# Kernel tuning notes

Hardware: AMD Instinct MI355X
Metric: run time of the kernel (lower is better)

Reference implementation:

```python
import jax, jax.numpy as jnp
import numpy as np

EMBED = 128
VOCAB = 64


def setup_inputs() -> dict:
    key = jax.random.key(0)
    ks = jax.random.split(key, 7)
    B, L, V, E = 512, 1024, VOCAB, EMBED
    seq = jax.random.normal(ks[0], (B, L, V), dtype=jnp.float32)
    # Linear params (torch convention: weight [out, in])
    W_in = jax.random.normal(ks[1], (E, V), dtype=jnp.float32) / np.sqrt(V)
    b_in = jax.random.normal(ks[2], (E,), dtype=jnp.float32) * 0.01
    W_h = jax.random.normal(ks[3], (E, 2 * E), dtype=jnp.float32) / np.sqrt(2 * E)
    b_h = jax.random.normal(ks[4], (E,), dtype=jnp.float32) * 0.01
    W_out = jax.random.normal(ks[5], (V, E), dtype=jnp.float32) / np.sqrt(E)
    b_out = jax.random.normal(ks[6], (V,), dtype=jnp.float32) * 0.01
    return {"seq": seq, "W_in": W_in, "b_in": b_in, "W_h": W_h,
            "b_h": b_h, "W_out": W_out, "b_out": b_out}


def reference(seq, W_in, b_in, W_h, b_h, W_out, b_out):
    B, L, V = seq.shape
    E = W_in.shape[0]
    # Precompute input projection for all timesteps (equivalent to per-step _in)
    x_proj = jnp.einsum('blv,ev->ble', seq, W_in) + b_in  # [B, L, E]
    # concat([x, h]) @ W_h.T == x @ W_h[:, :E].T + h @ W_h[:, E:].T
    Wh_x = W_h[:, :E].T  # [E, E]
    Wh_h = W_h[:, E:].T  # [E, E]

    def step(h, x_t):
        h_new = jax.nn.relu(x_t @ Wh_x + h @ Wh_h + b_h)
        return h_new, None

    h0 = jnp.zeros((B, E), dtype=seq.dtype)
    xs = jnp.swapaxes(x_proj, 0, 1)  # [L, B, E]
    h_final, _ = jax.lax.scan(step, h0, xs)
    return h_final @ W_out.T + b_out  # [B, V]
```

## Files before the change

kernel.cpp:

```cpp
#include <hip/hip_runtime.h>
#include <hip/hip_bf16.h>

namespace {
constexpr int Bn = 512;
constexpr int Ln = 1024;
constexpr int Vn = 64;
constexpr int En = 128;
constexpr int Kc = Vn + En;
constexpr size_t SEQB_BYTES  = (size_t)Bn * Ln * Vn * 2;
constexpr size_t WALLB_BYTES = (size_t)En * Kc * 2;
constexpr size_t BC_BYTES    = En * 4;
constexpr size_t WOUTP_BYTES = (size_t)Vn * En * 2;
constexpr size_t FAST_WS  = SEQB_BYTES + WALLB_BYTES + BC_BYTES;
constexpr size_t FAST_WS2 = SEQB_BYTES + WALLB_BYTES + BC_BYTES + WOUTP_BYTES;
}

typedef __attribute__((ext_vector_type(8))) short bf16x8;
typedef __attribute__((ext_vector_type(4))) float f32x4;
typedef __attribute__((ext_vector_type(8))) unsigned short u16x8;

__device__ __forceinline__ unsigned f2b(float f) {
  unsigned u = __float_as_uint(f);
  u += 0x7fffu + ((u >> 16) & 1u);
  return u >> 16;
}
__device__ __forceinline__ float b2f(unsigned short b) {
  return __uint_as_float(((unsigned)b) << 16);
}
__device__ __forceinline__ bf16x8 pack8(const float* v) {
  bf16x8 r;
#pragma unroll
  for (int i = 0; i < 8; ++i) r[i] = (short)f2b(v[i]);
  return r;
}

__device__ __forceinline__ int cm4(int kk) {
  return 32 * (kk >> 5) + 16 * ((kk >> 2) & 1) + 4 * ((kk >> 3) & 3) + (kk & 3);
}

#define MFMA __builtin_amdgcn_mfma_f32_16x16x32_bf16


__global__ void seq_cvt(const float* __restrict__ seq, unsigned short* __restrict__ seqb) {
  const size_t n = (size_t)Bn * Ln * Vn;
  size_t i = ((size_t)blockIdx.x * blockDim.x + threadIdx.x) * 8;
  const size_t stride = (size_t)gridDim.x * blockDim.x * 8;
  for (; i < n; i += stride) {
    const f32x4 a = *(const f32x4*)(seq + i);
    const f32x4 b = *(const f32x4*)(seq + i + 4);
    u16x8 o;
#pragma unroll
    for (int j = 0; j < 4; ++j) o[j] = (unsigned short)f2b(a[j]);
#pragma unroll
    for (int j = 0; j < 4; ++j) o[4 + j] = (unsigned short)f2b(b[j]);
    *(u16x8*)(seqb + i) = o;
  }
}

__global__ void rnn_setup2(const float* __restrict__ W_in, const float* __restrict__ b_in,
                           const float* __restrict__ W_h, const float* __restrict__ b_h,
                           unsigned short* __restrict__ wall2, float* __restrict__ bc) {
  const int j = blockIdx.x;
  const int k = threadIdx.x;
  const float* whr = W_h + j * (2 * En);
  float s;
  if (k < Vn) {
    s = 0.f;
#pragma unroll 8
    for (int e = 0; e < En; ++e) s = fmaf(W_in[e * Vn + k], whr[e], s);
  } else {
    s = whr[En + cm4(k - Vn)];
  }
  wall2[j * Kc + k] = (unsigned short)f2b(s);
  if (k == 0) {
    float b = b_h[j];
    for (int e = 0; e < En; ++e) b = fmaf(b_in[e], whr[e], b);
    bc[j] = b;
  }
}

__global__ void wout_setup(const float* __restrict__ W_out, unsigned short* __restrict__ woutp) {
  const int v = blockIdx.x;
  const int kk = threadIdx.x;
  woutp[v * En + kk] = (unsigned short)f2b(W_out[(size_t)v * En + cm4(kk)]);
}

__global__ __launch_bounds__(256, 1) void rnn_quad(
    const unsigned short* __restrict__ seqb, const unsigned short* __restrict__ wall2,
    const float* __restrict__ bc, const unsigned short* __restrict__ woutp,
    const float* __restrict__ b_out, float* __restrict__ out) {
  __shared__ __align__(16) unsigned char zlds[2][4][1024];

  const int tid = threadIdx.x;
  const int w   = tid >> 6;
  const int l   = tid & 63;
  const int l15 = l & 15;
  const int lg  = l >> 4;
  const int r0  = blockIdx.x * 16;

  bf16x8 Aw[2][6];
#pragma unroll
  for (int nn = 0; nn < 2; ++nn) {
    const unsigned short* row = wall2 + (size_t)(16 * (2 * w + nn) + l15) * Kc + lg * 8;
    Aw[nn][0] = *(const bf16x8*)(row);
    Aw[nn][1] = *(const bf16x8*)(row + 32);
#pragma unroll
    for (int p = 0; p < 4; ++p)
      Aw[nn][2 + p] = *(const bf16x8*)(row + Vn + 32 * ((w + p) & 3));
  }
  const f32x4 bcv0 = *(const f32x4*)(bc + 32 * w + 4 * lg);
  const f32x4 bcv1 = *(const f32x4*)(bc + 32 * w + 16 + 4 * lg);

  const int ro  = l * 16;
  const unsigned char* rA1 = &zlds[0][(w + 1) & 3][ro];
  const unsigned char* rA2 = &zlds[0][(w + 2) & 3][ro];
  const unsigned char* rA3 = &zlds[0][(w + 3) & 3][ro];
  const unsigned char* rB1 = &zlds[1][(w + 1) & 3][ro];
  const unsigned char* rB2 = &zlds[1][(w + 2) & 3][ro];
  const unsigned char* rB3 = &zlds[1][(w + 3) & 3][ro];
  unsigned char* wA = &zlds[0][w][ro];
  unsigned char* wB = &zlds[1][w][ro];

  for (int i = tid; i < 2048; i += 256) ((unsigned int*)zlds)[i] = 0u;
  bf16x8 zown;
#pragma unroll
  for (int i = 0; i < 8; ++i) zown[i] = 0;

  const unsigned short* sqb = seqb + ((size_t)(r0 + l15) * Ln) * Vn + lg * 8;
  bf16x8 sreg[4][2];

#define SEQ_PF(BI, T)                                                \
  { const int tp = ((T) < Ln) ? (T) : (Ln - 1);                      \
    const bf16x8* sp = (const bf16x8*)(sqb + (size_t)tp * Vn);       \
    sreg[BI][0] = sp[0];                                             \
    sreg[BI][1] = sp[4]; }

  SEQ_PF(0, 0)
  SEQ_PF(1, 1)
  SEQ_PF(2, 2)
  __syncthreads();

#define PHASE(P, R1, R2, R3, WR)                                              \
  {                                                                           \
    const bf16x8 zf1 = *(const bf16x8*)(R1);                                  \
    const bf16x8 zf2 = *(const bf16x8*)(R2);                                  \
    const bf16x8 zf3 = *(const bf16x8*)(R3);                                  \
    SEQ_PF(((P) + 3) & 3, t + (P) + 3);                                       \
    const bf16x8 s0 = sreg[(P)][0], s1 = sreg[(P)][1];                        \
       \
    f32x4 p0 = MFMA(Aw[0][0], s0, bcv0, 0, 0, 0);                             \
    f32x4 p1 = MFMA(Aw[1][0], s0, bcv1, 0, 0, 0);                             \
    f32x4 q0 = {0.f, 0.f, 0.f, 0.f}, q1 = {0.f, 0.f, 0.f, 0.f};               \
    q0 = MFMA(Aw[0][1], s1, q0, 0, 0, 0);                                     \
    q1 = MFMA(Aw[1][1], s1, q1, 0, 0, 0);                                     \
    p0 = MFMA(Aw[0][2], zown, p0, 0, 0, 0);                                   \
    p1 = MFMA(Aw[1][2], zown, p1, 0, 0, 0);                                   \
    q0 = MFMA(Aw[0][3], zf1, q0, 0, 0, 0);                                    \
    q1 = MFMA(Aw[1][3], zf1, q1, 0, 0, 0);                                    \
    p0 = MFMA(Aw[0][4], zf2, p0, 0, 0, 0);                                    \
    p1 = MFMA(Aw[1][4], zf2, p1, 0, 0, 0);                                    \
    q0 = MFMA(Aw[0][5], zf3, q0, 0, 0, 0);                                    \
    q1 = MFMA(Aw[1][5], zf3, q1, 0, 0, 0);                                    \
    const f32x4 a0 = p0 + q0, a1 = p1 + q1;                                   \
    const float x0 = fmaxf(a0[0], 0.f), x1 = fmaxf(a0[1], 0.f);               \
    const float x2 = fmaxf(a0[2], 0.f), x3 = fmaxf(a0[3], 0.f);               \
    const float y0 = fmaxf(a1[0], 0.f), y1 = fmaxf(a1[1], 0.f);               \
    const float y2 = fmaxf(a1[2], 0.f), y3 = fmaxf(a1[3], 0.f);               \
    unsigned u0, u1, u2, u3;                                                  \
    asm("v_cvt_pk_bf16_f32 %0, %1, %2" : "=v"(u0) : "v"(x0), "v"(x1));        \
    asm("v_cvt_pk_bf16_f32 %0, %1, %2" : "=v"(u1) : "v"(x2), "v"(x3));        \
    asm("v_cvt_pk_bf16_f32 %0, %1, %2" : "=v"(u2) : "v"(y0), "v"(y1));        \
    asm("v_cvt_pk_bf16_f32 %0, %1, %2" : "=v"(u3) : "v"(y2), "v"(y3));        \
    union { unsigned u[4]; bf16x8 v; } zc;                                    \
    zc.u[0] = u0; zc.u[1] = u1; zc.u[2] = u2; zc.u[3] = u3;                   \
    zown = zc.v;                                                              \
    *(bf16x8*)(WR) = zown;                                                    \
    asm volatile("s_waitcnt lgkmcnt(0)" ::: "memory");                        \
    __builtin_amdgcn_s_barrier();                                             \
    asm volatile("" ::: "memory");                                            \
  }

#pragma unroll 1
  for (int t = 0; t < Ln; t += 4) {
    PHASE(0, rA1, rA2, rA3, wB)
    PHASE(1, rB1, rB2, rB3, wA)
    PHASE(2, rA1, rA2, rA3, wB)
    PHASE(3, rB1, rB2, rB3, wA)
  }
#undef PHASE
#undef SEQ_PF

  {
    const bf16x8 zf1 = *(const bf16x8*)(rA1);
    const bf16x8 zf2 = *(const bf16x8*)(rA2);
    const bf16x8 zf3 = *(const bf16x8*)(rA3);
    const unsigned short* wrow = woutp + (size_t)(16 * w + l15) * En + lg * 8;
    f32x4 o = *(const f32x4*)(b_out + 16 * w + 4 * lg);
    o = MFMA(*(const bf16x8*)(wrow + 32 * w), zown, o, 0, 0, 0);
    o = MFMA(*(const bf16x8*)(wrow + 32 * ((w + 1) & 3)), zf1, o, 0, 0, 0);
    o = MFMA(*(const bf16x8*)(wrow + 32 * ((w + 2) & 3)), zf2, o, 0, 0, 0);
    o = MFMA(*(const bf16x8*)(wrow + 32 * ((w + 3) & 3)), zf3, o, 0, 0, 0);
    *(f32x4*)&out[(size_t)(r0 + l15) * Vn + 16 * w + 4 * lg] = o;
  }
}


__global__ void rnn_setup_bf(const float* __restrict__ W_in, const float* __restrict__ b_in,
                             const float* __restrict__ W_h, const float* __restrict__ b_h,
                             unsigned short* __restrict__ wallb, float* __restrict__ bc) {
  const int j = blockIdx.x;
  const int k = threadIdx.x;
  const float* whr = W_h + j * (2 * En);
  float s;
  if (k < Vn) {
    s = 0.f;
#pragma unroll 8
    for (int e = 0; e < En; ++e) s = fmaf(W_in[e * Vn + k], whr[e], s);
  } else {
    s = whr[Vn + k];
  }
  wallb[j * Kc + k] = (unsigned short)f2b(s);
  if (k == 0) {
    float b = b_h[j];
    for (int e = 0; e < En; ++e) b = fmaf(b_in[e], whr[e], b);
    bc[j] = b;
  }
}

__global__ __launch_bounds__(128, 1) void rnn_fast2(
    const unsigned short* __restrict__ seqb, const unsigned short* __restrict__ wallb,
    const float* __restrict__ bc, const float* __restrict__ W_out,
    const float* __restrict__ b_out, float* __restrict__ out) {
  __shared__ __align__(16) unsigned char hbB[2][4096];

  const int tid = threadIdx.x;
  const int w   = tid >> 6;
  const int l   = tid & 63;
  const int l15 = l & 15;
  const int lg  = l >> 4;
  const int r0  = blockIdx.x * 16;
  const int swz = (l15 & 7) << 4;

  bf16x8 Aw[4][6];
  f32x4 bcv[4];
#pragma unroll
  for (int nn = 0; nn < 4; ++nn) {
    const int n = 4 * w + nn;
    const unsigned short* p = wallb + (size_t)(16 * n + l15) * Kc + lg * 8;
#pragma unroll
    for (int kt = 0; kt < 6; ++kt) Aw[nn][kt] = *(const bf16x8*)(p + kt * 32);
    bcv[nn] = *(const f32x4*)(bc + 16 * n + 4 * lg);
  }

  for (int i = tid; i < 2048; i += 128) ((unsigned int*)hbB)[i] = 0u;

  const unsigned short* sqb = seqb + ((size_t)(r0 + l15) * Ln) * Vn + lg * 8;
  bf16x8 sreg[4][2];

#define SEQ_PF(BI, T)                                                \
  { const int tp = ((T) < Ln) ? (T) : (Ln - 1);                      \
    const bf16x8* sp = (const bf16x8*)(sqb + (size_t)tp * Vn);       \
    sreg[BI][0] = sp[0];                                             \
    sreg[BI][1] = sp[4]; }

  SEQ_PF(0, 0)
  SEQ_PF(1, 1)
  SEQ_PF(2, 2)
  __syncthreads();

#define PHASE(P)                                                               \
  {                                                                            \
    const int cb = (P) & 1;                                                    \
    const unsigned char* zb = hbB[cb] + l15 * 256;                             \
    const bf16x8 z0 = *(const bf16x8*)(zb + ((16 * lg) ^ swz));                \
    const bf16x8 z1 = *(const bf16x8*)(zb + ((64 + 16 * lg) ^ swz));           \
    const bf16x8 z2 = *(const bf16x8*)(zb + ((128 + 16 * lg) ^ swz));          \
    const bf16x8 z3 = *(const bf16x8*)(zb + ((192 + 16 * lg) ^ swz));          \
    SEQ_PF(((P) + 3) & 3, t + (P) + 3);                                        \
    const bf16x8 s0 = sreg[(P)][0], s1 = sreg[(P)][1];                         \
    f32x4 p0 = bcv[0], p1 = bcv[1], p2 = bcv[2], p3 = bcv[3];                  \
    f32x4 q0 = {0.f, 0.f, 0.f, 0.f}, q1 = {0.f, 0.f, 0.f, 0.f};                \
    f32x4 q2 = {0.f, 0.f, 0.f, 0.f}, q3 = {0.f, 0.f, 0.f, 0.f};                \
    p0 = MFMA(Aw[0][0], s0, p0, 0, 0, 0);                                      \
    p1 = MFMA(Aw[1][0], s0, p1, 0, 0, 0);                                      \
    p2 = MFMA(Aw[2][0], s0, p2, 0, 0, 0);                                      \
    p3 = MFMA(Aw[3][0], s0, p3, 0, 0, 0);                                      \
    q0 = MFMA(Aw[0][1], s1, q0, 0, 0, 0);                                      \
    q1 = MFMA(Aw[1][1], s1, q1, 0, 0, 0);                                      \
    q2 = MFMA(Aw[2][1], s1, q2, 0, 0, 0);                                      \
    q3 = MFMA(Aw[3][1], s1, q3, 0, 0, 0);                                      \
    p0 = MFMA(Aw[0][2], z0, p0, 0, 0, 0);                                      \
    p1 = MFMA(Aw[1][2], z0, p1, 0, 0, 0);                                      \
    p2 = MFMA(Aw[2][2], z0, p2, 0, 0, 0);                                      \
    p3 = MFMA(Aw[3][2], z0, p3, 0, 0, 0);                                      \
    q0 = MFMA(Aw[0][3], z1, q0, 0, 0, 0);                                      \
    q1 = MFMA(Aw[1][3], z1, q1, 0, 0, 0);                                      \
    q2 = MFMA(Aw[2][3], z1, q2, 0, 0, 0);                                      \
    q3 = MFMA(Aw[3][3], z1, q3, 0, 0, 0);                                      \
    p0 = MFMA(Aw[0][4], z2, p0, 0, 0, 0);                                      \
    p1 = MFMA(Aw[1][4], z2, p1, 0, 0, 0);                                      \
    p2 = MFMA(Aw[2][4], z2, p2, 0, 0, 0);                                      \
    p3 = MFMA(Aw[3][4], z2, p3, 0, 0, 0);                                      \
    q0 = MFMA(Aw[0][5], z3, q0, 0, 0, 0);                                      \
    q1 = MFMA(Aw[1][5], z3, q1, 0, 0, 0);                                      \
    q2 = MFMA(Aw[2][5], z3, q2, 0, 0, 0);                                      \
    q3 = MFMA(Aw[3][5], z3, q3, 0, 0, 0);                                      \
    unsigned char* wbB = hbB[cb ^ 1] + l15 * 256;                              \
    _Pragma("unroll") for (int nn = 0; nn < 4; ++nn) {                         \
      const f32x4 pp = (nn == 0) ? p0 : (nn == 1) ? p1 : (nn == 2) ? p2 : p3;  \
      const f32x4 qq = (nn == 0) ? q0 : (nn == 1) ? q1 : (nn == 2) ? q2 : q3;  \
      const float r0v = fmaxf(pp[0] + qq[0], 0.f);                             \
      const float r1v = fmaxf(pp[1] + qq[1], 0.f);                             \
      const float r2v = fmaxf(pp[2] + qq[2], 0.f);                             \
      const float r3v = fmaxf(pp[3] + qq[3], 0.f);                             \
      unsigned d0, d1;                                                         \
      asm("v_cvt_pk_bf16_f32 %0, %1, %2" : "=v"(d0) : "v"(r0v), "v"(r1v));     \
      asm("v_cvt_pk_bf16_f32 %0, %1, %2" : "=v"(d1) : "v"(r2v), "v"(r3v));     \
      uint2 dd; dd.x = d0; dd.y = d1;                                          \
      *(uint2*)(wbB + ((128 * w + 32 * nn + 8 * lg) ^ swz)) = dd;              \
    }                                                                          \
    asm volatile("s_waitcnt lgkmcnt(0)" ::: "memory");                         \
    __builtin_amdgcn_s_barrier();                                              \
    asm volatile("" ::: "memory");                                             \
  }

#pragma unroll 1
  for (int t = 0; t < Ln; t += 4) {
    PHASE(0)
    PHASE(1)
    PHASE(2)
    PHASE(3)
  }
#undef PHASE
#undef SEQ_PF

  bf16x8 hz[4];
  const unsigned char* zb0 = hbB[0] + l15 * 256;
#pragma unroll
  for (int kt = 0; kt < 4; ++kt)
    hz[kt] = *(const bf16x8*)(zb0 + ((64 * kt + 16 * lg) ^ swz));
#pragma unroll
  for (int m = 0; m < 2; ++m) {
    const int v = 16 * (2 * w + m) + l15;
    const float* wor = W_out + (size_t)v * En + lg * 8;
    const float bo = b_out[v];
    f32x4 oa = {bo, bo, bo, bo};
#pragma unroll
    for (int kt = 0; kt < 4; ++kt) {
      float tmp[8];
      const float* p = wor + kt * 32;
#pragma unroll
      for (int i = 0; i < 8; ++i) tmp[i] = p[i];
      oa = MFMA(hz[kt], pack8(tmp), oa, 0, 0, 0);
    }
#pragma unroll
    for (int i = 0; i < 4; ++i)
      out[(size_t)(r0 + 4 * lg + i) * Vn + v] = oa[i];
  }
}


__global__ __launch_bounds__(256, 1) void rnn_mfma(
    const float* __restrict__ seq, const float* __restrict__ W_in,
    const float* __restrict__ b_in, const float* __restrict__ W_h,
    const float* __restrict__ b_h, const float* __restrict__ W_out,
    const float* __restrict__ b_out, float* __restrict__ out) {
  __shared__ __align__(16) unsigned short hb[2][16][136];

  const int tid = threadIdx.x;
  const int w   = tid >> 6;
  const int l   = tid & 63;
  const int l15 = l & 15;
  const int lg  = l >> 4;
  const int r0  = blockIdx.x * 16;

  bf16x8 Bw[2][6];
  float bc[2];
#pragma unroll
  for (int n = 0; n < 2; ++n) {
    const int j = 32 * w + 16 * n + l15;
    const float* whr = W_h + j * (2 * En);
    float b = b_h[j];
    for (int e = 0; e < En; ++e) b = fmaf(b_in[e], whr[e], b);
    bc[n] = b;
#pragma unroll
    for (int kt = 0; kt < 6; ++kt) {
      float v[8];
#pragma unroll
      for (int i = 0; i < 8; ++i) {
        const int k = kt * 32 + lg * 8 + i;
        if (k < Vn) {
          float s = 0.f;
          for (int e = 0; e < En; ++e) s = fmaf(W_in[e * Vn + k], whr[e], s);
          v[i] = s;
        } else {
          v[i] = whr[Vn + k];
        }
      }
      Bw[n][kt] = pack8(v);
    }
  }

  for (int i = tid; i < 2 * 16 * 136; i += 256) ((unsigned short*)hb)[i] = 0;

  const float* sq = seq + ((size_t)(r0 + l15) * Ln) * Vn + lg * 8;
  f32x4 sbuf[4][4];

#define SEQ_PF(BI, T)                                                 \
  { const int tp = ((T) < Ln) ? (T) : (Ln - 1);                       \
    const f32x4* p0 = (const f32x4*)(sq + (size_t)tp * Vn);           \
    const f32x4* p1 = (const f32x4*)(sq + (size_t)tp * Vn + 32);      \
    sbuf[BI][0] = p0[0]; sbuf[BI][1] = p0[1];                         \
    sbuf[BI][2] = p1[0]; sbuf[BI][3] = p1[1]; }

  SEQ_PF(0, 0)
  SEQ_PF(1, 1)
  SEQ_PF(2, 2)
  __syncthreads();

#define PHASE(P)                                                              \
  {                                                                           \
    const int cb = (P) & 1, nb = cb ^ 1;                                      \
    const bf16x8 h0 = *(const bf16x8*)&hb[cb][l15][lg * 8];                   \
    const bf16x8 h1 = *(const bf16x8*)&hb[cb][l15][32 + lg * 8];              \
    const bf16x8 h2 = *(const bf16x8*)&hb[cb][l15][64 + lg * 8];              \
    const bf16x8 h3 = *(const bf16x8*)&hb[cb][l15][96 + lg * 8];              \
    SEQ_PF(((P) + 3) & 3, t + (P) + 3);                                       \
    float v0[8], v1[8];                                                       \
    _Pragma("unroll") for (int i = 0; i < 4; ++i) {                           \
      v0[i] = sbuf[(P)][0][i]; v0[4 + i] = sbuf[(P)][1][i];                   \
      v1[i] = sbuf[(P)][2][i]; v1[4 + i] = sbuf[(P)][3][i];                   \
    }                                                                         \
    const bf16x8 a0 = pack8(v0), a1 = pack8(v1);                              \
    f32x4 p0a = {bc[0], bc[0], bc[0], bc[0]};                                 \
    f32x4 p1a = {bc[1], bc[1], bc[1], bc[1]};                                 \
    f32x4 q0a = {0.f, 0.f, 0.f, 0.f}, q1a = {0.f, 0.f, 0.f, 0.f};             \
    p0a = MFMA(a0, Bw[0][0], p0a, 0, 0, 0);                                   \
    p1a = MFMA(a0, Bw[1][0], p1a, 0, 0, 0);                                   \
    p0a = MFMA(a1, Bw[0][1], p0a, 0, 0, 0);                                   \
    p1a = MFMA(a1, Bw[1][1], p1a, 0, 0, 0);                                   \
    p0a = MFMA(h0, Bw[0][2], p0a, 0, 0, 0);                                   \
    p1a = MFMA(h0, Bw[1][2], p1a, 0, 0, 0);                                   \
    q0a = MFMA(h2, Bw[0][4], q0a, 0, 0, 0);                                   \
    q1a = MFMA(h2, Bw[1][4], q1a, 0, 0, 0);                                   \
    p0a = MFMA(h1, Bw[0][3], p0a, 0, 0, 0);                                   \
    p1a = MFMA(h1, Bw[1][3], p1a, 0, 0, 0);                                   \
    q0a = MFMA(h3, Bw[0][5], q0a, 0, 0, 0);                                   \
    q1a = MFMA(h3, Bw[1][5], q1a, 0, 0, 0);                                   \
    const int j0 = 32 * w + l15, j1 = j0 + 16, rr = 4 * lg;                   \
    _Pragma("unroll") for (int i = 0; i < 4; ++i) {                           \
      hb[nb][rr + i][j0] = (unsigned short)f2b(fmaxf(p0a[i] + q0a[i], 0.f));  \
      hb[nb][rr + i][j1] = (unsigned short)f2b(fmaxf(p1a[i] + q1a[i], 0.f));  \
    }                                                                         \
    asm volatile("s_waitcnt lgkmcnt(0)" ::: "memory");                        \
    __builtin_amdgcn_s_barrier();                                             \
    asm volatile("" ::: "memory");                                            \
  }

#pragma unroll 1
  for (int t = 0; t < Ln; t += 4) {
    PHASE(0)
    PHASE(1)
    PHASE(2)
    PHASE(3)
  }
#undef PHASE
#undef SEQ_PF

  const int orow = tid >> 4;
  const int oc   = (tid & 15) * 4;
  float o0 = b_out[oc], o1 = b_out[oc + 1], o2 = b_out[oc + 2], o3 = b_out[oc + 3];
  const float* w0 = W_out + (size_t)(oc + 0) * En;
  const float* w1 = W_out + (size_t)(oc + 1) * En;
  const float* w2 = W_out + (size_t)(oc + 2) * En;
  const float* w3 = W_out + (size_t)(oc + 3) * En;
#pragma unroll 8
  for (int k = 0; k < En; ++k) {
    const float hv = b2f(hb[0][orow][k]);
    o0 = fmaf(hv, w0[k], o0);
    o1 = fmaf(hv, w1[k], o1);
    o2 = fmaf(hv, w2[k], o2);
    o3 = fmaf(hv, w3[k], o3);
  }
  *(float4*)&out[(size_t)(r0 + orow) * Vn + oc] = make_float4(o0, o1, o2, o3);
}

extern "C" void kernel_launch(void* const* d_in, const int* in_sizes, int n_in,
                              void* d_out, int out_size, void* d_ws, size_t ws_size,
                              hipStream_t stream) {
  const float* seq   = (const float*)d_in[0];
  const float* W_in  = (const float*)d_in[1];
  const float* b_in  = (const float*)d_in[2];
  const float* W_h   = (const float*)d_in[3];
  const float* b_h   = (const float*)d_in[4];
  const float* W_out = (const float*)d_in[5];
  const float* b_out = (const float*)d_in[6];
  float* out = (float*)d_out;

  if (ws_size >= FAST_WS2) {
    unsigned short* seqb  = (unsigned short*)d_ws;
    unsigned short* wall2 = (unsigned short*)((char*)d_ws + SEQB_BYTES);
    float* bc             = (float*)((char*)d_ws + SEQB_BYTES + WALLB_BYTES);
    unsigned short* woutp = (unsigned short*)((char*)d_ws + SEQB_BYTES + WALLB_BYTES + BC_BYTES);
    seq_cvt<<<2048, 256, 0, stream>>>(seq, seqb);
    rnn_setup2<<<En, Kc, 0, stream>>>(W_in, b_in, W_h, b_h, wall2, bc);
    wout_setup<<<Vn, En, 0, stream>>>(W_out, woutp);
    rnn_quad<<<Bn / 16, 256, 0, stream>>>(seqb, wall2, bc, woutp, b_out, out);
  } else if (ws_size >= FAST_WS) {
    unsigned short* seqb  = (unsigned short*)d_ws;
    unsigned short* wallb = (unsigned short*)((char*)d_ws + SEQB_BYTES);
    float* bc = (float*)((char*)d_ws + SEQB_BYTES + WALLB_BYTES);
    seq_cvt<<<2048, 256, 0, stream>>>(seq, seqb);
    rnn_setup_bf<<<En, Kc, 0, stream>>>(W_in, b_in, W_h, b_h, wallb, bc);
    rnn_fast2<<<Bn / 16, 128, 0, stream>>>(seqb, wallb, bc, W_out, b_out, out);
  } else {
    rnn_mfma<<<Bn / 16, 256, 0, stream>>>(seq, W_in, b_in, W_h, b_h, W_out, b_out, out);
  }
}
```

Before: 281.2 us.

## Precompute input projection for all timesteps in a parallel pre-pass

Adds a fully parallel sp_pre kernel that converts seq to bf16 and multiplies it by the folded input weights plus bias for every timestep. The result is stored in a layout matched to the recurrent kernel's MFMA fragments. The new rnn_sp recurrence then only does the hidden-state MFMAs, with one 16-byte load per lane per step instead of two loads and two MFMAs on seq. This moves work off the serial critical path. The cost is a larger workspace (B*L*E bf16, twice the size of the seq bf16 copy) and twice the intermediate memory traffic. It also removes the older rnn_fast2 fallback path.

```diff
diff --git a/kernel.cpp b/kernel.cpp
--- a/kernel.cpp
+++ b/kernel.cpp
@@ -8,11 +8,13 @@
 constexpr int En = 128;
 constexpr int Kc = Vn + En;
 constexpr size_t SEQB_BYTES  = (size_t)Bn * Ln * Vn * 2;
+constexpr size_t SP_BYTES    = (size_t)Bn * Ln * En * 2;
 constexpr size_t WALLB_BYTES = (size_t)En * Kc * 2;
 constexpr size_t BC_BYTES    = En * 4;
 constexpr size_t WOUTP_BYTES = (size_t)Vn * En * 2;
 constexpr size_t FAST_WS  = SEQB_BYTES + WALLB_BYTES + BC_BYTES;
 constexpr size_t FAST_WS2 = SEQB_BYTES + WALLB_BYTES + BC_BYTES + WOUTP_BYTES;
+constexpr size_t SP_WS    = SP_BYTES + WALLB_BYTES + BC_BYTES + WOUTP_BYTES;
 }
 
 typedef __attribute__((ext_vector_type(8))) short bf16x8;
@@ -85,6 +87,173 @@
   woutp[v * En + kk] = (unsigned short)f2b(W_out[(size_t)v * En + cm4(kk)]);
 }
 
+__global__ __launch_bounds__(256) void sp_pre(
+    const float* __restrict__ seq, const unsigned short* __restrict__ wall2,
+    const float* __restrict__ bc, unsigned short* __restrict__ sp) {
+  const int tid = threadIdx.x;
+  const int w   = tid >> 6;
+  const int l   = tid & 63;
+  const int l15 = l & 15;
+  const int lg  = l >> 4;
+  const int g   = blockIdx.x >> 5;
+  const int tc  = blockIdx.x & 31;
+  const int row = g * 16 + l15;
+
+  bf16x8 A00, A01, A10, A11;
+  {
+    const unsigned short* rp0 = wall2 + (size_t)(16 * (2 * w) + l15) * Kc + lg * 8;
+    const unsigned short* rp1 = wall2 + (size_t)(16 * (2 * w + 1) + l15) * Kc + lg * 8;
+    A00 = *(const bf16x8*)(rp0);
+    A01 = *(const bf16x8*)(rp0 + 32);
+    A10 = *(const bf16x8*)(rp1);
+    A11 = *(const bf16x8*)(rp1 + 32);
+  }
+  const f32x4 bcv0 = *(const f32x4*)(bc + 32 * w + 4 * lg);
+  const f32x4 bcv1 = *(const f32x4*)(bc + 32 * w + 16 + 4 * lg);
+
+  const float* sq = seq + ((size_t)row * Ln) * Vn + lg * 8;
+#pragma unroll 4
+  for (int tt = 0; tt < 32; ++tt) {
+    const int t = tc * 32 + tt;
+    const float* s4 = sq + (size_t)t * Vn;
+    float v0[8], v1[8];
+    const f32x4 a = *(const f32x4*)(s4);
+    const f32x4 b = *(const f32x4*)(s4 + 4);
+    const f32x4 c = *(const f32x4*)(s4 + 32);
+    const f32x4 d = *(const f32x4*)(s4 + 36);
+#pragma unroll
+    for (int i = 0; i < 4; ++i) { v0[i] = a[i]; v0[4 + i] = b[i]; v1[i] = c[i]; v1[4 + i] = d[i]; }
+    const bf16x8 s0 = pack8(v0), s1 = pack8(v1);
+    f32x4 p0 = MFMA(A00, s0, bcv0, 0, 0, 0);
+    p0 = MFMA(A01, s1, p0, 0, 0, 0);
+    f32x4 p1 = MFMA(A10, s0, bcv1, 0, 0, 0);
+    p1 = MFMA(A11, s1, p1, 0, 0, 0);
+    unsigned u0, u1, u2, u3;
+    asm("v_cvt_pk_bf16_f32 %0, %1, %2" : "=v"(u0) : "v"(p0[0]), "v"(p0[1]));
+    asm("v_cvt_pk_bf16_f32 %0, %1, %2" : "=v"(u1) : "v"(p0[2]), "v"(p0[3]));
+    asm("v_cvt_pk_bf16_f32 %0, %1, %2" : "=v"(u2) : "v"(p1[0]), "v"(p1[1]));
+    asm("v_cvt_pk_bf16_f32 %0, %1, %2" : "=v"(u3) : "v"(p1[2]), "v"(p1[3]));
+    union { unsigned u[4]; u16x8 v; } o;
+    o.u[0] = u0; o.u[1] = u1; o.u[2] = u2; o.u[3] = u3;
+    const size_t idx = ((((size_t)t * Bn + row) * 4 + w) * 4 + lg) * 8;
+    *(u16x8*)(sp + idx) = o.v;
+  }
+}
+
+__global__ __launch_bounds__(256, 1) void rnn_sp(
+    const unsigned short* __restrict__ sp, const unsigned short* __restrict__ wall2,
+    const unsigned short* __restrict__ woutp, const float* __restrict__ b_out,
+    float* __restrict__ out) {
+  __shared__ __align__(16) unsigned char zb[2][4][1024];
+
+  const int tid = threadIdx.x;
+  const int w   = tid >> 6;
+  const int l   = tid & 63;
+  const int l15 = l & 15;
+  const int lg  = l >> 4;
+  const int r0  = blockIdx.x * 16;
+
+  bf16x8 Awz[2][4];
+#pragma unroll
+  for (int nn = 0; nn < 2; ++nn) {
+    const unsigned short* row = wall2 + (size_t)(16 * (2 * w + nn) + l15) * Kc + lg * 8;
+#pragma unroll
+    for (int p = 0; p < 4; ++p)
+      Awz[nn][p] = *(const bf16x8*)(row + Vn + 32 * ((w + p) & 3));
+  }
+
+  const int ro = l * 16;
+  const unsigned char* rA1 = &zb[0][(w + 1) & 3][ro];
+  const unsigned char* rA2 = &zb[0][(w + 2) & 3][ro];
+  const unsigned char* rA3 = &zb[0][(w + 3) & 3][ro];
+  const unsigned char* rB1 = &zb[1][(w + 1) & 3][ro];
+  const unsigned char* rB2 = &zb[1][(w + 2) & 3][ro];
+  const unsigned char* rB3 = &zb[1][(w + 3) & 3][ro];
+  unsigned char* wA = &zb[0][w][ro];
+  unsigned char* wB = &zb[1][w][ro];
+
+  for (int i = tid; i < 2048; i += 256) ((unsigned int*)zb)[i] = 0u;
+  bf16x8 zown;
+#pragma unroll
+  for (int i = 0; i < 8; ++i) zown[i] = 0;
+
+  const unsigned short* spl = sp + (((size_t)(r0 + l15) * 4 + w) * 4 + lg) * 8;
+  u16x8 spreg[4];
+
+#define SP_PF(BI, T)                                                  \
+  { const size_t tp = ((T) < Ln) ? (size_t)(T) : (size_t)(Ln - 1);    \
+    spreg[BI] = *(const u16x8*)(spl + tp * 65536); }
+
+  SP_PF(0, 0)
+  SP_PF(1, 1)
+  SP_PF(2, 2)
+  __syncthreads();
+
+#define PHASE(P, R1, R2, R3, WR)                                              \
+  {                                                                           \
+    const bf16x8 zf1 = *(const bf16x8*)(R1);                                  \
+    const bf16x8 zf2 = *(const bf16x8*)(R2);                                  \
+    const bf16x8 zf3 = *(const bf16x8*)(R3);                                  \
+    SP_PF(((P) + 3) & 3, t + (P) + 3);                                        \
+    const u16x8 sv = spreg[(P)];                                              \
+    f32x4 p0, p1;                                                             \
+    p0[0] = b2f(sv[0]); p0[1] = b2f(sv[1]);                                   \
+    p0[2] = b2f(sv[2]); p0[3] = b2f(sv[3]);                                   \
+    p1[0] = b2f(sv[4]); p1[1] = b2f(sv[5]);                                   \
+    p1[2] = b2f(sv[6]); p1[3] = b2f(sv[7]);                                   \
+    f32x4 q0 = {0.f, 0.f, 0.f, 0.f}, q1 = {0.f, 0.f, 0.f, 0.f};               \
+    p0 = MFMA(Awz[0][0], zown, p0, 0, 0, 0);                                  \
+    p1 = MFMA(Awz[1][0], zown, p1, 0, 0, 0);                                  \
+    q0 = MFMA(Awz[0][1], zf1, q0, 0, 0, 0);                                   \
+    q1 = MFMA(Awz[1][1], zf1, q1, 0, 0, 0);                                   \
+    p0 = MFMA(Awz[0][2], zf2, p0, 0, 0, 0);                                   \
+    p1 = MFMA(Awz[1][2], zf2, p1, 0, 0, 0);                                   \
+    q0 = MFMA(Awz[0][3], zf3, q0, 0, 0, 0);                                   \
+    q1 = MFMA(Awz[1][3], zf3, q1, 0, 0, 0);                                   \
+    const f32x4 a0 = p0 + q0, a1 = p1 + q1;                                   \
+    const float x0 = fmaxf(a0[0], 0.f), x1 = fmaxf(a0[1], 0.f);               \
+    const float x2 = fmaxf(a0[2], 0.f), x3 = fmaxf(a0[3], 0.f);               \
+    const float y0 = fmaxf(a1[0], 0.f), y1 = fmaxf(a1[1], 0.f);               \
+    const float y2 = fmaxf(a1[2], 0.f), y3 = fmaxf(a1[3], 0.f);               \
+    unsigned u0, u1, u2, u3;                                                  \
+    asm("v_cvt_pk_bf16_f32 %0, %1, %2" : "=v"(u0) : "v"(x0), "v"(x1));        \
+    asm("v_cvt_pk_bf16_f32 %0, %1, %2" : "=v"(u1) : "v"(x2), "v"(x3));        \
+    asm("v_cvt_pk_bf16_f32 %0, %1, %2" : "=v"(u2) : "v"(y0), "v"(y1));        \
+    asm("v_cvt_pk_bf16_f32 %0, %1, %2" : "=v"(u3) : "v"(y2), "v"(y3));        \
+    union { unsigned u[4]; bf16x8 v; } zc;                                    \
+    zc.u[0] = u0; zc.u[1] = u1; zc.u[2] = u2; zc.u[3] = u3;                   \
+    zown = zc.v;                                                              \
+    *(bf16x8*)(WR) = zown;                                                    \
+    asm volatile("s_waitcnt lgkmcnt(0)" ::: "memory");                        \
+    __builtin_amdgcn_s_barrier();                                             \
+    asm volatile("" ::: "memory");                                            \
+  }
+
+#pragma unroll 1
+  for (int t = 0; t < Ln; t += 4) {
+    PHASE(0, rA1, rA2, rA3, wB)
+    PHASE(1, rB1, rB2, rB3, wA)
+    PHASE(2, rA1, rA2, rA3, wB)
+    PHASE(3, rB1, rB2, rB3, wA)
+  }
+#undef PHASE
+#undef SP_PF
+
+  {
+    const bf16x8 zf1 = *(const bf16x8*)(rA1);
+    const bf16x8 zf2 = *(const bf16x8*)(rA2);
+    const bf16x8 zf3 = *(const bf16x8*)(rA3);
+    const unsigned short* wrow = woutp + (size_t)(16 * w + l15) * En + lg * 8;
+    f32x4 o = *(const f32x4*)(b_out + 16 * w + 4 * lg);
+    o = MFMA(*(const bf16x8*)(wrow + 32 * w), zown, o, 0, 0, 0);
+    o = MFMA(*(const bf16x8*)(wrow + 32 * ((w + 1) & 3)), zf1, o, 0, 0, 0);
+    o = MFMA(*(const bf16x8*)(wrow + 32 * ((w + 2) & 3)), zf2, o, 0, 0, 0);
+    o = MFMA(*(const bf16x8*)(wrow + 32 * ((w + 3) & 3)), zf3, o, 0, 0, 0);
+    *(f32x4*)&out[(size_t)(r0 + l15) * Vn + 16 * w + 4 * lg] = o;
+  }
+}
+
+
 __global__ __launch_bounds__(256, 1) void rnn_quad(
     const unsigned short* __restrict__ seqb, const unsigned short* __restrict__ wall2,
     const float* __restrict__ bc, const unsigned short* __restrict__ woutp,
@@ -147,7 +316,6 @@
     const bf16x8 zf3 = *(const bf16x8*)(R3);                                  \
     SEQ_PF(((P) + 3) & 3, t + (P) + 3);                                       \
     const bf16x8 s0 = sreg[(P)][0], s1 = sreg[(P)][1];                        \
-       \
     f32x4 p0 = MFMA(Aw[0][0], s0, bcv0, 0, 0, 0);                             \
     f32x4 p1 = MFMA(Aw[1][0], s0, bcv1, 0, 0, 0);                             \
     f32x4 q0 = {0.f, 0.f, 0.f, 0.f}, q1 = {0.f, 0.f, 0.f, 0.f};               \
@@ -205,33 +373,12 @@
 }
 
 
-__global__ void rnn_setup_bf(const float* __restrict__ W_in, const float* __restrict__ b_in,
-                             const float* __restrict__ W_h, const float* __restrict__ b_h,
-                             unsigned short* __restrict__ wallb, float* __restrict__ bc) {
-  const int j = blockIdx.x;
-  const int k = threadIdx.x;
-  const float* whr = W_h + j * (2 * En);
-  float s;
-  if (k < Vn) {
-    s = 0.f;
-#pragma unroll 8
-    for (int e = 0; e < En; ++e) s = fmaf(W_in[e * Vn + k], whr[e], s);
-  } else {
-    s = whr[Vn + k];
-  }
-  wallb[j * Kc + k] = (unsigned short)f2b(s);
-  if (k == 0) {
-    float b = b_h[j];
-    for (int e = 0; e < En; ++e) b = fmaf(b_in[e], whr[e], b);
-    bc[j] = b;
-  }
-}
-
-__global__ __launch_bounds__(128, 1) void rnn_fast2(
-    const unsigned short* __restrict__ seqb, const unsigned short* __restrict__ wallb,
-    const float* __restrict__ bc, const float* __restrict__ W_out,
+__global__ __launch_bounds__(256, 1) void rnn_mfma(
+    const float* __restrict__ seq, const float* __restrict__ W_in,
+    const float* __restrict__ b_in, const float* __restrict__ W_h,
+    const float* __restrict__ b_h, const float* __restrict__ W_out,
     const float* __restrict__ b_out, float* __restrict__ out) {
-  __shared__ __align__(16) unsigned char hbB[2][4096];
+  __shared__ __align__(16) unsigned short hb[2][16][136];
 
   const int tid = threadIdx.x;
   const int w   = tid >> 6;
@@ -239,150 +386,16 @@
   const int l15 = l & 15;
   const int lg  = l >> 4;
   const int r0  = blockIdx.x * 16;
-  const int swz = (l15 & 7) << 4;
-
-  bf16x8 Aw[4][6];
-  f32x4 bcv[4];
-#pragma unroll
-  for (int nn = 0; nn < 4; ++nn) {
-    const int n = 4 * w + nn;
-    const unsigned short* p = wallb + (size_t)(16 * n + l15) * Kc + lg * 8;
-#pragma unroll
-    for (int kt = 0; kt < 6; ++kt) Aw[nn][kt] = *(const bf16x8*)(p + kt * 32);
-    bcv[nn] = *(const f32x4*)(bc + 16 * n + 4 * lg);
-  }
-
-  for (int i = tid; i < 2048; i += 128) ((unsigned int*)hbB)[i] = 0u;
-
-  const unsigned short* sqb = seqb + ((size_t)(r0 + l15) * Ln) * Vn + lg * 8;
-  bf16x8 sreg[4][2];
-
-#define SEQ_PF(BI, T)                                                \
-  { const int tp = ((T) < Ln) ? (T) : (Ln - 1);                      \
-    const bf16x8* sp = (const bf16x8*)(sqb + (size_t)tp * Vn);       \
-    sreg[BI][0] = sp[0];                                             \
-    sreg[BI][1] = sp[4]; }
-
-  SEQ_PF(0, 0)
-  SEQ_PF(1, 1)
-  SEQ_PF(2, 2)
-  __syncthreads();
-
-#define PHASE(P)                                                               \
-  {                                                                            \
-    const int cb = (P) & 1;                                                    \
-    const unsigned char* zb = hbB[cb] + l15 * 256;                             \
-    const bf16x8 z0 = *(const bf16x8*)(zb + ((16 * lg) ^ swz));                \
-    const bf16x8 z1 = *(const bf16x8*)(zb + ((64 + 16 * lg) ^ swz));           \
-    const bf16x8 z2 = *(const bf16x8*)(zb + ((128 + 16 * lg) ^ swz));          \
-    const bf16x8 z3 = *(const bf16x8*)(zb + ((192 + 16 * lg) ^ swz));          \
-    SEQ_PF(((P) + 3) & 3, t + (P) + 3);                                        \
-    const bf16x8 s0 = sreg[(P)][0], s1 = sreg[(P)][1];                         \
-    f32x4 p0 = bcv[0], p1 = bcv[1], p2 = bcv[2], p3 = bcv[3];                  \
-    f32x4 q0 = {0.f, 0.f, 0.f, 0.f}, q1 = {0.f, 0.f, 0.f, 0.f};                \
-    f32x4 q2 = {0.f, 0.f, 0.f, 0.f}, q3 = {0.f, 0.f, 0.f, 0.f};                \
-    p0 = MFMA(Aw[0][0], s0, p0, 0, 0, 0);                                      \
-    p1 = MFMA(Aw[1][0], s0, p1, 0, 0, 0);                                      \
-    p2 = MFMA(Aw[2][0], s0, p2, 0, 0, 0);                                      \
-    p3 = MFMA(Aw[3][0], s0, p3, 0, 0, 0);                                      \
-    q0 = MFMA(Aw[0][1], s1, q0, 0, 0, 0);                                      \
-    q1 = MFMA(Aw[1][1], s1, q1, 0, 0, 0);                                      \
-    q2 = MFMA(Aw[2][1], s1, q2, 0, 0, 0);                                      \
-    q3 = MFMA(Aw[3][1], s1, q3, 0, 0, 0);                                      \
-    p0 = MFMA(Aw[0][2], z0, p0, 0, 0, 0);                                      \
-    p1 = MFMA(Aw[1][2], z0, p1, 0, 0, 0);                                      \
-    p2 = MFMA(Aw[2][2], z0, p2, 0, 0, 0);                                      \
-    p3 = MFMA(Aw[3][2], z0, p3, 0, 0, 0);                                      \
-    q0 = MFMA(Aw[0][3], z1, q0, 0, 0, 0);                                      \
-    q1 = MFMA(Aw[1][3], z1, q1, 0, 0, 0);                                      \
-    q2 = MFMA(Aw[2][3], z1, q2, 0, 0, 0);                                      \
-    q3 = MFMA(Aw[3][3], z1, q3, 0, 0, 0);                                      \
-    p0 = MFMA(Aw[0][4], z2, p0, 0, 0, 0);                                      \
-    p1 = MFMA(Aw[1][4], z2, p1, 0, 0, 0);                                      \
-    p2 = MFMA(Aw[2][4], z2, p2, 0, 0, 0);                                      \
-    p3 = MFMA(Aw[3][4], z2, p3, 0, 0, 0);                                      \
-    q0 = MFMA(Aw[0][5], z3, q0, 0, 0, 0);                                      \
-    q1 = MFMA(Aw[1][5], z3, q1, 0, 0, 0);                                      \
-    q2 = MFMA(Aw[2][5], z3, q2, 0, 0, 0);                                      \
-    q3 = MFMA(Aw[3][5], z3, q3, 0, 0, 0);                                      \
-    unsigned char* wbB = hbB[cb ^ 1] + l15 * 256;                              \
-    _Pragma("unroll") for (int nn = 0; nn < 4; ++nn) {                         \
-      const f32x4 pp = (nn == 0) ? p0 : (nn == 1) ? p1 : (nn == 2) ? p2 : p3;  \
-      const f32x4 qq = (nn == 0) ? q0 : (nn == 1) ? q1 : (nn == 2) ? q2 : q3;  \
-      const float r0v = fmaxf(pp[0] + qq[0], 0.f);                             \
-      const float r1v = fmaxf(pp[1] + qq[1], 0.f);                             \
-      const float r2v = fmaxf(pp[2] + qq[2], 0.f);                             \
-      const float r3v = fmaxf(pp[3] + qq[3], 0.f);                             \
-      unsigned d0, d1;                                                         \
-      asm("v_cvt_pk_bf16_f32 %0, %1, %2" : "=v"(d0) : "v"(r0v), "v"(r1v));     \
-      asm("v_cvt_pk_bf16_f32 %0, %1, %2" : "=v"(d1) : "v"(r2v), "v"(r3v));     \
-      uint2 dd; dd.x = d0; dd.y = d1;                                          \
-      *(uint2*)(wbB + ((128 * w + 32 * nn + 8 * lg) ^ swz)) = dd;              \
-    }                                                                          \
-    asm volatile("s_waitcnt lgkmcnt(0)" ::: "memory");                         \
-    __builtin_amdgcn_s_barrier();                                              \
-    asm volatile("" ::: "memory");                                             \
-  }
-
-#pragma unroll 1
-  for (int t = 0; t < Ln; t += 4) {
-    PHASE(0)
-    PHASE(1)
-    PHASE(2)
-    PHASE(3)
-  }
-#undef PHASE
-#undef SEQ_PF
-
-  bf16x8 hz[4];
-  const unsigned char* zb0 = hbB[0] + l15 * 256;
-#pragma unroll
-  for (int kt = 0; kt < 4; ++kt)
-    hz[kt] = *(const bf16x8*)(zb0 + ((64 * kt + 16 * lg) ^ swz));
-#pragma unroll
-  for (int m = 0; m < 2; ++m) {
-    const int v = 16 * (2 * w + m) + l15;
-    const float* wor = W_out + (size_t)v * En + lg * 8;
-    const float bo = b_out[v];
-    f32x4 oa = {bo, bo, bo, bo};
-#pragma unroll
-    for (int kt = 0; kt < 4; ++kt) {
-      float tmp[8];
-      const float* p = wor + kt * 32;
-#pragma unroll
-      for (int i = 0; i < 8; ++i) tmp[i] = p[i];
-      oa = MFMA(hz[kt], pack8(tmp), oa, 0, 0, 0);
-    }
-#pragma unroll
-    for (int i = 0; i < 4; ++i)
-      out[(size_t)(r0 + 4 * lg + i) * Vn + v] = oa[i];
-  }
-}
-
-
-__global__ __launch_bounds__(256, 1) void rnn_mfma(
-    const float* __restrict__ seq, const float* __restrict__ W_in,
-    const float* __restrict__ b_in, const float* __restrict__ W_h,
-    const float* __restrict__ b_h, const float* __restrict__ W_out,
-    const float* __restrict__ b_out, float* __restrict__ out) {
-  __shared__ __align__(16) unsigned short hb[2][16][136];
-
-  const int tid = threadIdx.x;
-  const int w   = tid >> 6;
-  const int l   = tid & 63;
-  const int l15 = l & 15;
-  const int lg  = l >> 4;
-  const int r0  = blockIdx.x * 16;
 
   bf16x8 Bw[2][6];
-  float bc[2];
+  float bcl[2];
 #pragma unroll
   for (int n = 0; n < 2; ++n) {
     const int j = 32 * w + 16 * n + l15;
     const float* whr = W_h + j * (2 * En);
     float b = b_h[j];
     for (int e = 0; e < En; ++e) b = fmaf(b_in[e], whr[e], b);
-    bc[n] = b;
+    bcl[n] = b;
 #pragma unroll
     for (int kt = 0; kt < 6; ++kt) {
       float v[8];
@@ -432,8 +445,8 @@
       v1[i] = sbuf[(P)][2][i]; v1[4 + i] = sbuf[(P)][3][i];                   \
     }                                                                         \
     const bf16x8 a0 = pack8(v0), a1 = pack8(v1);                              \
-    f32x4 p0a = {bc[0], bc[0], bc[0], bc[0]};                                 \
-    f32x4 p1a = {bc[1], bc[1], bc[1], bc[1]};                                 \
+    f32x4 p0a = {bcl[0], bcl[0], bcl[0], bcl[0]};                             \
+    f32x4 p1a = {bcl[1], bcl[1], bcl[1], bcl[1]};                             \
     f32x4 q0a = {0.f, 0.f, 0.f, 0.f}, q1a = {0.f, 0.f, 0.f, 0.f};             \
     p0a = MFMA(a0, Bw[0][0], p0a, 0, 0, 0);                                   \
     p1a = MFMA(a0, Bw[1][0], p1a, 0, 0, 0);                                   \
@@ -497,7 +510,16 @@
   const float* b_out = (const float*)d_in[6];
   float* out = (float*)d_out;
 
-  if (ws_size >= FAST_WS2) {
+  if (ws_size >= SP_WS) {
+    unsigned short* sp    = (unsigned short*)d_ws;
+    unsigned short* wall2 = (unsigned short*)((char*)d_ws + SP_BYTES);
+    float* bc             = (float*)((char*)d_ws + SP_BYTES + WALLB_BYTES);
+    unsigned short* woutp = (unsigned short*)((char*)d_ws + SP_BYTES + WALLB_BYTES + BC_BYTES);
+    rnn_setup2<<<En, Kc, 0, stream>>>(W_in, b_in, W_h, b_h, wall2, bc);
+    wout_setup<<<Vn, En, 0, stream>>>(W_out, woutp);
+    sp_pre<<<1024, 256, 0, stream>>>(seq, wall2, bc, sp);
+    rnn_sp<<<Bn / 16, 256, 0, stream>>>(sp, wall2, woutp, b_out, out);
+  } else if (ws_size >= FAST_WS2) {
     unsigned short* seqb  = (unsigned short*)d_ws;
     unsigned short* wall2 = (unsigned short*)((char*)d_ws + SEQB_BYTES);
     float* bc             = (float*)((char*)d_ws + SEQB_BYTES + WALLB_BYTES);
@@ -506,13 +528,6 @@
     rnn_setup2<<<En, Kc, 0, stream>>>(W_in, b_in, W_h, b_h, wall2, bc);
     wout_setup<<<Vn, En, 0, stream>>>(W_out, woutp);
     rnn_quad<<<Bn / 16, 256, 0, stream>>>(seqb, wall2, bc, woutp, b_out, out);
-  } else if (ws_size >= FAST_WS) {
-    unsigned short* seqb  = (unsigned short*)d_ws;
-    unsigned short* wallb = (unsigned short*)((char*)d_ws + SEQB_BYTES);
-    float* bc = (float*)((char*)d_ws + SEQB_BYTES + WALLB_BYTES);
-    seq_cvt<<<2048, 256, 0, stream>>>(seq, seqb);
-    rnn_setup_bf<<<En, Kc, 0, stream>>>(W_in, b_in, W_h, b_h, wallb, bc);
-    rnn_fast2<<<Bn / 16, 128, 0, stream>>>(seqb, wallb, bc, W_out, b_out, out);
   } else {
     rnn_mfma<<<Bn / 16, 256, 0, stream>>>(seq, W_in, b_in, W_h, b_h, W_out, b_out, out);
   }
```

Measured after the change: 338.5 us. +20.4%, slower.
